# Performance work log

Measured on AMD Instinct MI355X. Metric: run time of the kernel, lower is better.

Reference implementation:

```python
import jax, jax.numpy as jnp
import numpy as np

B, N, HL, D, HID, O, E, S, K = 8, 64, 32, 256, 1024, 256, 8, 3, 2


def setup_inputs() -> dict:
    key = jax.random.key(0)
    ks = jax.random.split(key, 12)
    w = 0.02
    return {
        "feature_vectors": jax.random.normal(ks[0], (B, N, HL, D), dtype=jnp.float32),
        "object_types": jax.random.uniform(ks[1], (B, N, HL, S, 1), dtype=jnp.float32),
        "gate_w": jax.random.normal(ks[2], (D, E), dtype=jnp.float32) * w,
        "gate_b": jnp.zeros((E,), dtype=jnp.float32),
        "shared_w1": jax.random.normal(ks[3], (S, D, HID), dtype=jnp.float32) * w,
        "shared_b1": jnp.zeros((S, HID), dtype=jnp.float32),
        "shared_w2": jax.random.normal(ks[4], (S, HID, O), dtype=jnp.float32) * w,
        "shared_b2": jnp.zeros((S, O), dtype=jnp.float32),
        "ind_w1": jax.random.normal(ks[5], (E, D, HID), dtype=jnp.float32) * w,
        "ind_b1": jnp.zeros((E, HID), dtype=jnp.float32),
        "ind_w2": jax.random.normal(ks[6], (E, HID, O), dtype=jnp.float32) * w,
        "ind_b2": jnp.zeros((E, O), dtype=jnp.float32),
    }


def reference(feature_vectors, object_types, gate_w, gate_b,
              shared_w1, shared_b1, shared_w2, shared_b2,
              ind_w1, ind_b1, ind_w2, ind_b2):
    b, n, hl, d = feature_vectors.shape
    x = feature_vectors.reshape(-1, d)                      # (T, D)
    T = x.shape[0]

    # gating: softmax -> top-k -> renormalize selected probs
    gates = jax.nn.softmax(x @ gate_w + gate_b, axis=-1)    # (T, E)
    vals, idx = jax.lax.top_k(gates, K)                     # (T, K)
    w = vals / vals.sum(axis=-1, keepdims=True)
    # dense (T, E) combine weights: zero outside top-k, equivalent to scatter-add loop
    w_full = jnp.zeros_like(gates).at[jnp.arange(T)[:, None], idx].set(w)

    # shared experts: all S experts on every token, weighted by object_types
    sh_h = jax.nn.relu(jnp.einsum('td,sdh->tsh', x, shared_w1) + shared_b1)
    sh_o = jnp.einsum('tsh,sho->tso', sh_h, shared_w2) + shared_b2  # (T, S, O)
    obj = object_types.reshape(-1, S, 1)                    # (T, S, 1)
    shared_out = (sh_o * obj).sum(axis=1)                   # (T, O)

    # independent experts: dense all-expert GEMM, combined by masked gate weights
    ih = jax.nn.relu(jnp.einsum('td,edh->teh', x, ind_w1) + ind_b1)
    io = jnp.einsum('teh,eho->teo', ih, ind_w2) + ind_b2    # (T, E, O)
    ind_out = jnp.einsum('te,teo->to', w_full, io)          # (T, O)

    out = 0.5 * shared_out + 0.5 * ind_out
    return out.reshape(b, n, hl, -1)
```

## Files before the change

kernel.cpp:

```cpp
#include <hip/hip_runtime.h>
#include <hip/hip_bf16.h>
#include <stdint.h>

#define TOK   16384
#define DIM   256
#define HIDN  1024
#define OUTD  256
#define NEXP  8
#define NSH   3
#define NSLOT 11
#define TM    64
#define NCH   32
#define HSTR  40

typedef short bf16x8  __attribute__((ext_vector_type(8)));
typedef float f32x4   __attribute__((ext_vector_type(4)));
typedef float f32x16  __attribute__((ext_vector_type(16)));
typedef short short4v __attribute__((ext_vector_type(4)));

constexpr size_t XB_OFF   = 0;
constexpr size_t W1P_OFF  = XB_OFF  + (size_t)TOK*DIM*2;
constexpr size_t W2P_OFF  = W1P_OFF + (size_t)NSLOT*DIM*HIDN*2;
constexpr size_t WTS_OFF  = W2P_OFF + (size_t)NSLOT*HIDN*OUTD*2;
constexpr size_t IDS_OFF  = WTS_OFF + (size_t)TOK*2*4;
constexpr size_t CNT_OFF  = IDS_OFF + (size_t)TOK*2*4;
constexpr size_t LTOK_OFF = CNT_OFF + 256;
constexpr size_t LW_OFF   = LTOK_OFF + (size_t)NEXP*TOK*4;
constexpr size_t WS_NEED  = LW_OFF + (size_t)NEXP*TOK*4;

__device__ __forceinline__ unsigned short f2bf(float f) {
    __hip_bfloat16 h = __float2bfloat16(f);
    return *reinterpret_cast<unsigned short*>(&h);
}

__device__ __forceinline__ f32x4 mfma16(bf16x8 a, bf16x8 b, f32x4 c) {
    return __builtin_amdgcn_mfma_f32_16x16x32_bf16(a, b, c, 0, 0, 0);
}
__device__ __forceinline__ f32x16 mfma32(bf16x8 a, bf16x8 b, f32x16 c) {
    return __builtin_amdgcn_mfma_f32_32x32x16_bf16(a, b, c, 0, 0, 0);
}

__device__ __forceinline__ void gload_lds16(const void* g, void* l) {
    __builtin_amdgcn_global_load_lds(
        (const __attribute__((address_space(1))) unsigned int*)g,
        (__attribute__((address_space(3))) unsigned int*)l, 16, 0, 0);
}

__device__ __forceinline__ void fence_sched() { __builtin_amdgcn_sched_barrier(0); }

__global__ __launch_bounds__(256) void k_prep(
    const float* __restrict__ x, const float* __restrict__ gw,
    const float* __restrict__ gb, short* __restrict__ xb,
    float* __restrict__ wts, int* __restrict__ ids) {
    int wid = threadIdx.x >> 6, lane = threadIdx.x & 63;
    int t = blockIdx.x * 4 + wid;
    const float* xr = x + (size_t)t * DIM;
    {
        float4 v = reinterpret_cast<const float4*>(xr)[lane];
        short4v o;
        o[0] = (short)f2bf(v.x); o[1] = (short)f2bf(v.y);
        o[2] = (short)f2bf(v.z); o[3] = (short)f2bf(v.w);
        reinterpret_cast<short4v*>(xb + (size_t)t * DIM)[lane] = o;
    }
    float acc[NEXP] = {0.f,0.f,0.f,0.f,0.f,0.f,0.f,0.f};
    #pragma unroll
    for (int i = 0; i < DIM/64; ++i) {
        int d = i*64 + lane;
        float xv = xr[d];
        const float* g = gw + (size_t)d * NEXP;
        #pragma unroll
        for (int e = 0; e < NEXP; ++e) acc[e] = fmaf(xv, g[e], acc[e]);
    }
    #pragma unroll
    for (int off = 32; off; off >>= 1) {
        #pragma unroll
        for (int e = 0; e < NEXP; ++e) acc[e] += __shfl_xor(acc[e], off, 64);
    }
    if (lane == 0) {
        float l[NEXP];
        #pragma unroll
        for (int e = 0; e < NEXP; ++e) l[e] = acc[e] + gb[e];
        int e0 = 0; float v0 = l[0];
        #pragma unroll
        for (int e = 1; e < NEXP; ++e) if (l[e] > v0) { v0 = l[e]; e0 = e; }
        int e1 = -1; float v1 = -1e30f;
        #pragma unroll
        for (int e = 0; e < NEXP; ++e) if (e != e0 && l[e] > v1) { v1 = l[e]; e1 = e; }
        float r = expf(v1 - v0);
        float w0 = 0.5f / (1.f + r);
        float w1 = 0.5f * r / (1.f + r);
        ids[2*t]   = e0;  ids[2*t+1] = e1;
        wts[2*t]   = w0;  wts[2*t+1] = w1;
    }
}

__global__ __launch_bounds__(256) void k_convert_w(
    const float* __restrict__ sw1, const float* __restrict__ iw1,
    const float* __restrict__ sw2, const float* __restrict__ iw2,
    short* __restrict__ w1p, short* __restrict__ w2p) {
    __shared__ float tile[32][68];
    int bid = blockIdx.x, tid = threadIdx.x;
    const int W1B = NSLOT * 8 * 16;
    bool isW1 = bid < W1B;
    int b = isW1 ? bid : bid - W1B;
    int NTG = isW1 ? 16 : 4;
    int KT  = isW1 ? 8 : 32;
    int Nd  = isW1 ? HIDN : OUTD;
    int ntg = b % NTG; b /= NTG;
    int kt  = b % KT;
    int slot = b / KT;
    const float* src;
    if (isW1) src = (slot < NSH) ? sw1 + (size_t)slot*DIM*HIDN  : iw1 + (size_t)(slot-NSH)*DIM*HIDN;
    else      src = (slot < NSH) ? sw2 + (size_t)slot*HIDN*OUTD : iw2 + (size_t)(slot-NSH)*HIDN*OUTD;
    {
        int tr = tid >> 3, tc = (tid & 7) * 8;
        const float* s = src + (size_t)(kt*32 + tr)*Nd + ntg*64 + tc;
        float4 v0 = *reinterpret_cast<const float4*>(s);
        float4 v1 = *reinterpret_cast<const float4*>(s + 4);
        *reinterpret_cast<float4*>(&tile[tr][tc])     = v0;
        *reinterpret_cast<float4*>(&tile[tr][tc + 4]) = v1;
    }
    __syncthreads();
    if (isW1) {
        int ntl = tid >> 6, lane = tid & 63;
        int n  = ntl*16 + (lane & 15);
        int k8 = (lane >> 4) * 8;
        bf16x8 o;
        #pragma unroll
        for (int j = 0; j < 8; ++j) o[j] = (short)f2bf(tile[k8 + j][n]);
        size_t gidx = (((size_t)slot*8 + kt)*64 + ntg*4 + ntl)*64 + lane;
        reinterpret_cast<bf16x8*>(w1p)[gidx] = o;
    } else {
        int sub = tid >> 6, lane = tid & 63;
        int kt_sub = sub >> 1, nt_sub = sub & 1;
        int n  = nt_sub*32 + (lane & 31);
        int k8 = kt_sub*16 + (lane >> 5) * 8;
        bf16x8 o;
        #pragma unroll
        for (int j = 0; j < 8; ++j) o[j] = (short)f2bf(tile[k8 + j][n]);
        size_t gidx = (((size_t)slot*64 + kt*2 + kt_sub)*8 + ntg*2 + nt_sub)*64 + lane;
        reinterpret_cast<bf16x8*>(w2p)[gidx] = o;
    }
}

__global__ __launch_bounds__(256) void k_route(
    const int* __restrict__ ids, const float* __restrict__ wts,
    int* __restrict__ cnt, int* __restrict__ ltok, float* __restrict__ lw) {
    __shared__ int lcnt[NEXP];
    __shared__ int gbase[NEXP];
    int tid = threadIdx.x;
    if (tid < NEXP) lcnt[tid] = 0;
    __syncthreads();
    int t = blockIdx.x * 256 + tid;
    int e0 = ids[2*t], e1 = ids[2*t+1];
    int p0 = atomicAdd(&lcnt[e0], 1);
    int p1 = atomicAdd(&lcnt[e1], 1);
    __syncthreads();
    if (tid < NEXP) gbase[tid] = atomicAdd(&cnt[tid], lcnt[tid]);
    __syncthreads();
    size_t o0 = (size_t)e0*TOK + gbase[e0] + p0;
    size_t o1 = (size_t)e1*TOK + gbase[e1] + p1;
    ltok[o0] = t;  lw[o0] = wts[2*t];
    ltok[o1] = t;  lw[o1] = wts[2*t+1];
}

__global__ __launch_bounds__(512) void k_moe(
    const short* __restrict__ xb, const short* __restrict__ w1p, const short* __restrict__ w2p,
    const float* __restrict__ sb1, const float* __restrict__ sb2,
    const float* __restrict__ ib1, const float* __restrict__ ib2,
    const float* __restrict__ obj, const int* __restrict__ cnt,
    const int* __restrict__ ltok, const float* __restrict__ lw,
    float* __restrict__ out)
{
    __shared__ __align__(16) char Wb1[2][16384];
    __shared__ __align__(16) short Hs[TM * HSTR];
    __shared__ float bias_lds[HIDN];
    __shared__ int   tokl[TM];
    __shared__ float twl[TM];

    const int slot = blockIdx.y;
    const int m0   = blockIdx.x * TM;
    const bool sh  = slot < NSH;
    const int e    = slot - NSH;
    int count = TOK;
    if (!sh) { count = cnt[e]; if (m0 >= count) return; }

    const int tid  = threadIdx.x;
    const int w    = tid >> 6, lane = tid & 63;
    const int wm   = w >> 1,   wn   = w & 1;
    const int pmr  = w & 1,    pnc  = w >> 1;
    const int lrow = lane & 15, g   = lane >> 4;
    const int l31  = lane & 31, hi  = lane >> 5;

    if (tid < TM) {
        if (sh) {
            tokl[tid] = m0 + tid;
            twl[tid]  = 0.5f * obj[(size_t)(m0 + tid)*NSH + slot];
        } else {
            int p = m0 + tid;
            bool ok = p < count;
            tokl[tid] = ok ? ltok[(size_t)e*TOK + p] : 0;
            twl[tid]  = ok ? lw[(size_t)e*TOK + p] : 0.f;
        }
    }
    __syncthreads();

    const char* w1base = (const char*)w1p;
    const char* w2base = (const char*)w2p;
    const float* b1v = sh ? (sb1 + slot*HIDN) : (ib1 + (size_t)e*HIDN);

    const int tokA = tokl[wm*16 + lrow];
    bf16x8 areg[8];
    #pragma unroll
    for (int kt = 0; kt < 8; ++kt)
        areg[kt] = *reinterpret_cast<const bf16x8*>(
            xb + (size_t)tokA*DIM + kt*32 + g*8);

    if (w < 4)
        gload_lds16((const char*)b1v + w*1024 + lane*16, (char*)bias_lds + w*1024);

    auto stage_w1 = [&](int c, int buf) {
        #pragma unroll
        for (int i = 0; i < 2; ++i)
            gload_lds16(
                w1base + ((((size_t)slot*8 + w)*64 + c*2 + i) << 10) + lane*16,
                Wb1[buf] + ((w*2 + i) << 10));
    };

    asm volatile("s_waitcnt vmcnt(0) lgkmcnt(0)" ::: "memory");
    __syncthreads();

    stage_w1(0, 0);
    stage_w1(1, 1);

    f32x16 acc2[2] = {};
    for (int c = 0; c < NCH; ++c) {
        const int p = c & 1;
        if (c + 1 < NCH) { fence_sched(); asm volatile("s_waitcnt vmcnt(2)" ::: "memory"); }
        else             { fence_sched(); asm volatile("s_waitcnt vmcnt(0)" ::: "memory"); }
        fence_sched();
        __builtin_amdgcn_s_barrier();
        fence_sched();

        f32x4 acc1 = {};
        #pragma unroll
        for (int kt = 0; kt < 8; ++kt) {
            bf16x8 b = *reinterpret_cast<const bf16x8*>(
                Wb1[p] + ((kt*2 + wn) << 10) + lane*16);
            acc1 = mfma16(areg[kt], b, acc1);
        }
        {
            int col = wn*16 + lrow;
            float bias = bias_lds[c*32 + col];
            #pragma unroll
            for (int r = 0; r < 4; ++r) {
                int row = wm*16 + g*4 + r;
                float v = fmaxf(acc1[r] + bias, 0.f) * twl[row];
                Hs[row*HSTR + col] = (short)f2bf(v);
            }
        }
        fence_sched();
        asm volatile("s_waitcnt lgkmcnt(0)" ::: "memory");
        fence_sched();
        __builtin_amdgcn_s_barrier();
        fence_sched();

        if (c + 2 < NCH) stage_w1(c + 2, p);
        fence_sched();

        {
            bf16x8 wf[2][2];
            #pragma unroll
            for (int ks = 0; ks < 2; ++ks)
                #pragma unroll
                for (int j = 0; j < 2; ++j)
                    wf[ks][j] = *reinterpret_cast<const bf16x8*>(
                        w2base + ((((size_t)slot*64 + c*2 + ks)*8 + pnc*2 + j) << 10) + lane*16);
            #pragma unroll
            for (int ks = 0; ks < 2; ++ks) {
                bf16x8 av = *reinterpret_cast<const bf16x8*>(
                    Hs + (pmr*32 + l31)*HSTR + ks*16 + hi*8);
                acc2[0] = mfma32(av, wf[ks][0], acc2[0]);
                acc2[1] = mfma32(av, wf[ks][1], acc2[1]);
            }
        }
        fence_sched();
        asm volatile("s_waitcnt lgkmcnt(0)" ::: "memory");
        fence_sched();
        __builtin_amdgcn_s_barrier();
        fence_sched();
    }

    {
        const float* b2 = sh ? (sb2 + slot*OUTD) : (ib2 + (size_t)e*OUTD);
        #pragma unroll
        for (int j = 0; j < 2; ++j) {
            int col = pnc*64 + j*32 + l31;
            float b2v = b2[col];
            #pragma unroll
            for (int r = 0; r < 16; ++r) {
                int row = pmr*32 + (r & 3) + 8*(r >> 2) + 4*hi;
                if (sh || (m0 + row < count)) {
                    int t = tokl[row];
                    float v = acc2[j][r] + twl[row] * b2v;
                    atomicAdd(&out[(size_t)t*OUTD + col], v);
                }
            }
        }
    }
}

extern "C" void kernel_launch(void* const* d_in, const int* in_sizes, int n_in,
                              void* d_out, int out_size, void* d_ws, size_t ws_size,
                              hipStream_t stream) {
    const float* x   = (const float*)d_in[0];
    const float* obj = (const float*)d_in[1];
    const float* gw  = (const float*)d_in[2];
    const float* gb  = (const float*)d_in[3];
    const float* sw1 = (const float*)d_in[4];
    const float* sb1 = (const float*)d_in[5];
    const float* sw2 = (const float*)d_in[6];
    const float* sb2 = (const float*)d_in[7];
    const float* iw1 = (const float*)d_in[8];
    const float* ib1 = (const float*)d_in[9];
    const float* iw2 = (const float*)d_in[10];
    const float* ib2 = (const float*)d_in[11];
    float* out = (float*)d_out;
    char* ws = (char*)d_ws;
    if (ws_size < WS_NEED) return;

    short* xb   = (short*)(ws + XB_OFF);
    short* w1p  = (short*)(ws + W1P_OFF);
    short* w2p  = (short*)(ws + W2P_OFF);
    float* wts  = (float*)(ws + WTS_OFF);
    int*   ids  = (int*)  (ws + IDS_OFF);
    int*   cnt  = (int*)  (ws + CNT_OFF);
    int*   ltok = (int*)  (ws + LTOK_OFF);
    float* lwt  = (float*)(ws + LW_OFF);

    hipMemsetAsync(ws + CNT_OFF, 0, 256, stream);
    hipMemsetAsync(out, 0, (size_t)out_size * 4, stream);
    k_prep<<<TOK/4, 256, 0, stream>>>(x, gw, gb, xb, wts, ids);
    k_convert_w<<<NSLOT*8*16 + NSLOT*32*4, 256, 0, stream>>>(sw1, iw1, sw2, iw2, w1p, w2p);
    k_route<<<TOK/256, 256, 0, stream>>>(ids, wts, cnt, ltok, lwt);
    k_moe<<<dim3(TOK/TM, NSLOT), 512, 0, stream>>>(
        xb, w1p, w2p, sb1, sb2, ib1, ib2, obj, cnt, ltok, lwt, out);
}
```

Before: 217.4 us.

## Software-pipeline GEMM1 and GEMM2 stages with double-buffered hidden tile

Restructures the per-chunk loop so each iteration computes the first-layer tile for chunk s while running the second-layer MFMAs for chunk s-1, using a double-buffered Hs in LDS. This cuts the barriers per chunk from three to one. W1 staging now prefetches only one chunk ahead, and each iteration waits on vmcnt(0), so the outstanding global loads (including the W2 fragment loads) are fully drained at every barrier. That may expose load latency that the previous two-deep prefetch hid.

New measurement: 215.2 us. Within noise of the previous version (-1.0%).

```diff
diff --git a/kernel.cpp b/kernel.cpp
--- a/kernel.cpp
+++ b/kernel.cpp
@@ -173,7 +173,7 @@
     float* __restrict__ out)
 {
     __shared__ __align__(16) char Wb1[2][16384];
-    __shared__ __align__(16) short Hs[TM * HSTR];
+    __shared__ __align__(16) short Hs[2][TM * HSTR];
     __shared__ float bias_lds[HIDN];
     __shared__ int   tokl[TM];
     __shared__ float twl[TM];
@@ -231,64 +231,53 @@
     __syncthreads();
 
     stage_w1(0, 0);
-    stage_w1(1, 1);
 
     f32x16 acc2[2] = {};
-    for (int c = 0; c < NCH; ++c) {
-        const int p = c & 1;
-        if (c + 1 < NCH) { fence_sched(); asm volatile("s_waitcnt vmcnt(2)" ::: "memory"); }
-        else             { fence_sched(); asm volatile("s_waitcnt vmcnt(0)" ::: "memory"); }
+    for (int s = 0; s <= NCH; ++s) {
+        fence_sched();
+        asm volatile("s_waitcnt vmcnt(0) lgkmcnt(0)" ::: "memory");
         fence_sched();
         __builtin_amdgcn_s_barrier();
         fence_sched();
-
-        f32x4 acc1 = {};
-        #pragma unroll
-        for (int kt = 0; kt < 8; ++kt) {
-            bf16x8 b = *reinterpret_cast<const bf16x8*>(
-                Wb1[p] + ((kt*2 + wn) << 10) + lane*16);
-            acc1 = mfma16(areg[kt], b, acc1);
-        }
-        {
+        if (s + 1 < NCH) stage_w1(s + 1, (s + 1) & 1);
+
+        if (s < NCH) {
+            f32x4 acc1 = {};
+            #pragma unroll
+            for (int kt = 0; kt < 8; ++kt) {
+                bf16x8 b = *reinterpret_cast<const bf16x8*>(
+                    Wb1[s & 1] + ((kt*2 + wn) << 10) + lane*16);
+                acc1 = mfma16(areg[kt], b, acc1);
+            }
             int col = wn*16 + lrow;
-            float bias = bias_lds[c*32 + col];
+            float bias = bias_lds[s*32 + col];
+            short* hb = Hs[s & 1];
             #pragma unroll
             for (int r = 0; r < 4; ++r) {
                 int row = wm*16 + g*4 + r;
                 float v = fmaxf(acc1[r] + bias, 0.f) * twl[row];
-                Hs[row*HSTR + col] = (short)f2bf(v);
+                hb[row*HSTR + col] = (short)f2bf(v);
             }
         }
-        fence_sched();
-        asm volatile("s_waitcnt lgkmcnt(0)" ::: "memory");
-        fence_sched();
-        __builtin_amdgcn_s_barrier();
-        fence_sched();
-
-        if (c + 2 < NCH) stage_w1(c + 2, p);
-        fence_sched();
-
-        {
+
+        if (s >= 1) {
+            const int d = s - 1;
+            const short* hb = Hs[d & 1];
             bf16x8 wf[2][2];
             #pragma unroll
             for (int ks = 0; ks < 2; ++ks)
                 #pragma unroll
                 for (int j = 0; j < 2; ++j)
                     wf[ks][j] = *reinterpret_cast<const bf16x8*>(
-                        w2base + ((((size_t)slot*64 + c*2 + ks)*8 + pnc*2 + j) << 10) + lane*16);
+                        w2base + ((((size_t)slot*64 + d*2 + ks)*8 + pnc*2 + j) << 10) + lane*16);
             #pragma unroll
             for (int ks = 0; ks < 2; ++ks) {
                 bf16x8 av = *reinterpret_cast<const bf16x8*>(
-                    Hs + (pmr*32 + l31)*HSTR + ks*16 + hi*8);
+                    hb + (pmr*32 + l31)*HSTR + ks*16 + hi*8);
                 acc2[0] = mfma32(av, wf[ks][0], acc2[0]);
                 acc2[1] = mfma32(av, wf[ks][1], acc2[1]);
             }
         }
-        fence_sched();
-        asm volatile("s_waitcnt lgkmcnt(0)" ::: "memory");
-        fence_sched();
-        __builtin_amdgcn_s_barrier();
-        fence_sched();
     }
 
     {
```
